# Kernel tuning notes

Measured on AMD Instinct MI355X. Metric: run time of the kernel, lower is better.

The kernel has to match this reference:

```python
import jax, jax.numpy as jnp
import numpy as np

N, D, E = 50000, 128, 800000


def setup_inputs() -> dict:
    key = jax.random.key(0)
    ks = jax.random.split(key, 12)
    s = 1.0 / np.sqrt(D)
    return {
        "x": jax.random.normal(ks[0], (N, D), jnp.float32),
        "edge_index": jax.random.randint(ks[1], (2, E), 0, N, jnp.int32),
        "W1": jax.random.normal(ks[2], (D, D), jnp.float32) * s,
        "bc1": jnp.zeros((D,), jnp.float32),
        "W2": jax.random.normal(ks[3], (D, D), jnp.float32) * s,
        "bc2": jnp.zeros((D,), jnp.float32),
        "w11": jax.random.normal(ks[4], (D, D), jnp.float32) * s,
        "w12": jax.random.normal(ks[5], (D, D), jnp.float32) * s,
        "b1": jax.random.uniform(ks[6], (D,), jnp.float32, -s, s),
        "w21": jax.random.normal(ks[7], (D, D), jnp.float32) * s,
        "w22": jax.random.normal(ks[8], (D, D), jnp.float32) * s,
        "b2": jax.random.uniform(ks[9], (D,), jnp.float32, -s, s),
    }


def gcn_conv(x, W, b, src, dst):
    """PyG GCNConv: self-loops + symmetric D^-1/2 (A+I) D^-1/2 normalization."""
    n = x.shape[0]
    h = x @ W  # [N, D]
    ones = jnp.ones(dst.shape[0], h.dtype)
    deg = jax.ops.segment_sum(ones, dst, num_segments=n) + 1.0  # +1 for self-loop
    dinv = jax.lax.rsqrt(deg)
    norm = dinv[src] * dinv[dst]  # [E]
    agg = jax.ops.segment_sum(h[src] * norm[:, None], dst, num_segments=n)
    agg = agg + h * (dinv * dinv)[:, None]  # self-loop messages
    return agg + b


def reference(x, edge_index, W1, bc1, W2, bc2, w11, w12, b1, w21, w22, b2):
    src, dst = edge_index[0], edge_index[1]
    # layer 1: forward and reversed edge directions (dropout is identity in eval)
    o1 = jax.nn.relu(gcn_conv(x, W1, bc1, src, dst))
    o2 = jax.nn.relu(gcn_conv(x, W1, bc1, dst, src))
    G = jax.nn.sigmoid(o1 @ w11.T + o2 @ w12.T + b1)
    h = G * o1 + (1.0 - G) * o2
    # layer 2
    p1 = jax.nn.relu(gcn_conv(h, W2, bc2, src, dst))
    p2 = jax.nn.relu(gcn_conv(h, W2, bc2, dst, src))
    G2 = jax.nn.sigmoid(p1 @ w21.T + p2 @ w22.T + b2)
    return G2 * p1 + (1.0 - G2) * p2
```

## Files before the change

kernel.cpp:

```cpp
#include <hip/hip_runtime.h>
#include <hip/hip_bf16.h>
#include <hip/hip_fp16.h>
#include <math.h>

#define D 128
#define SEG 4096
#define BSH 7
#define RCAP 4096
#define ACAP 4096
#define TRS 133

typedef _Float16 half8  __attribute__((ext_vector_type(8)));
typedef _Float16 half4v __attribute__((ext_vector_type(4)));
typedef float    fx4    __attribute__((ext_vector_type(4)));

__global__ __launch_bounds__(256) void scat2_kernel(const int* __restrict__ src,
                                                    const int* __restrict__ dst,
                                                    int e, int nb,
                                                    int* __restrict__ gcur1, int* __restrict__ gcur2,
                                                    unsigned int* __restrict__ rec1,
                                                    unsigned int* __restrict__ rec2) {
    __shared__ int h1[512], h2[512], o1[512], o2[512], run1[512], run2[512];
    int tid = threadIdx.x;
    for (int b = tid; b < nb; b += 256) { h1[b] = 0; h2[b] = 0; run1[b] = 0; run2[b] = 0; }
    __syncthreads();
    int s0 = blockIdx.x * SEG;
    int s1 = min(e, s0 + SEG);
    for (int idx = s0 + tid; idx < s1; idx += 256) {
        atomicAdd(&h1[dst[idx] >> BSH], 1);
        atomicAdd(&h2[src[idx] >> BSH], 1);
    }
    __syncthreads();
    for (int b = tid; b < nb; b += 256) {
        o1[b] = atomicAdd(&gcur1[b], h1[b]);
        o2[b] = atomicAdd(&gcur2[b], h2[b]);
    }
    __syncthreads();
    for (int idx = s0 + tid; idx < s1; idx += 256) {
        unsigned int sv = (unsigned int)src[idx];
        unsigned int dv = (unsigned int)dst[idx];
        int b1 = dv >> BSH, b2 = sv >> BSH;
        int p1 = o1[b1] + atomicAdd(&run1[b1], 1);
        if (p1 < RCAP) rec1[(size_t)b1 * RCAP + p1] = (dv << 16) | sv;
        int p2 = o2[b2] + atomicAdd(&run2[b2], 1);
        if (p2 < RCAP) rec2[(size_t)b2 * RCAP + p2] = (sv << 16) | dv;
    }
}

__global__ __launch_bounds__(256) void fin_kernel(const unsigned int* __restrict__ rec1,
                                                  const unsigned int* __restrict__ rec2,
                                                  const int* __restrict__ gcur1, const int* __restrict__ gcur2,
                                                  unsigned short* __restrict__ adj1, unsigned short* __restrict__ adj2,
                                                  int* __restrict__ ip1, int* __restrict__ ipe1,
                                                  int* __restrict__ ip2, int* __restrict__ ipe2,
                                                  float* __restrict__ dinv1, float* __restrict__ dinv2,
                                                  int n) {
    __shared__ unsigned int Lrec[RCAP];
    __shared__ unsigned short sadj[ACAP];
    __shared__ int deg[128], pscan[128], cur[128];
    __shared__ int ptot_s;
    int bkt = blockIdx.x;
    int dir = blockIdx.y;
    const unsigned int* rec = dir ? rec2 : rec1;
    const int* gc = dir ? gcur2 : gcur1;
    unsigned short* adj = dir ? adj2 : adj1;
    int* ip  = dir ? ip2 : ip1;
    int* ipe = dir ? ipe2 : ipe1;
    float* dinv = dir ? dinv2 : dinv1;

    int tid = threadIdx.x;
    int cnt = gc[bkt];
    if (cnt > RCAP) cnt = RCAP;
    size_t rbase = (size_t)bkt * RCAP;
    if (tid < 128) { deg[tid] = 0; cur[tid] = 0; }
    for (int i = tid; i < cnt; i += 256) Lrec[i] = rec[rbase + i];
    __syncthreads();
    int base = bkt << BSH;
    for (int i = tid; i < cnt; i += 256)
        atomicAdd(&deg[(int)(Lrec[i] >> 16) - base], 1);
    __syncthreads();
    if (tid < 128) pscan[tid] = (deg[tid] + 7) & ~7;
    __syncthreads();
    #pragma unroll
    for (int st = 1; st < 128; st <<= 1) {
        int add = (tid < 128 && tid >= st) ? pscan[tid - st] : 0;
        __syncthreads();
        if (tid < 128) pscan[tid] += add;
        __syncthreads();
    }
    if (tid == 127) ptot_s = min(pscan[127], ACAP);
    __syncthreads();
    int ptot = ptot_s;
    for (int i = tid; i < ptot; i += 256) sadj[i] = (unsigned short)n;
    __syncthreads();
    for (int i = tid; i < cnt; i += 256) {
        unsigned int r = Lrec[i];
        int l = (int)(r >> 16) - base;
        int pd = (deg[l] + 7) & ~7;
        int pos = pscan[l] - pd + atomicAdd(&cur[l], 1);
        if (pos < ACAP) sadj[pos] = (unsigned short)(r & 0xffffu);
    }
    __syncthreads();
    int gbase = bkt * ACAP;
    for (int i = tid; i < ptot; i += 256) adj[gbase + i] = sadj[i];
    if (tid < 128) {
        int node = base + tid;
        if (node < n) {
            int pd = (deg[tid] + 7) & ~7;
            ip[node]  = gbase + pscan[tid] - pd;
            ipe[node] = gbase + pscan[tid];
            dinv[node] = rsqrtf((float)deg[tid] + 1.0f);
        }
    }
    if (bkt == 0 && tid == 200) dinv[n] = 0.0f;
}

__global__ __launch_bounds__(256) void prep_kernel(const float* __restrict__ W1, const float* __restrict__ W2,
                                                   const float* __restrict__ w11, const float* __restrict__ w12,
                                                   const float* __restrict__ w21, const float* __restrict__ w22,
                                                   _Float16* __restrict__ T1, _Float16* __restrict__ T2,
                                                   _Float16* __restrict__ o11, _Float16* __restrict__ o12,
                                                   _Float16* __restrict__ o21, _Float16* __restrict__ o22) {
    __shared__ float s[32][33];
    int which = blockIdx.y;
    if (which < 2) {
        const float* w = which ? W2 : W1;
        _Float16* t = which ? T2 : T1;
        int tk = (blockIdx.x >> 2) * 32;
        int tc = (blockIdx.x & 3) * 32;
        int lr = threadIdx.x >> 5;
        int lc = threadIdx.x & 31;
        #pragma unroll
        for (int i = 0; i < 32; i += 8)
            s[lr + i][lc] = w[(size_t)(tk + lr + i) * D + tc + lc];
        __syncthreads();
        #pragma unroll
        for (int i = 0; i < 32; i += 8)
            t[(size_t)(tc + lr + i) * D + tk + lc] = (_Float16)s[lc][lr + i];
    } else {
        int wsel = which - 2;
        const float* w = (wsel == 0) ? w11 : (wsel == 1) ? w12 : (wsel == 2) ? w21 : w22;
        _Float16* o = (wsel == 0) ? o11 : (wsel == 1) ? o12 : (wsel == 2) ? o21 : o22;
        int idx = (blockIdx.x * 256 + threadIdx.x) * 4;
        float4 v = *(const float4*)&w[idx];
        half4v h = {(_Float16)v.x, (_Float16)v.y, (_Float16)v.z, (_Float16)v.w};
        *(half4v*)&o[idx] = h;
    }
}

__global__ __launch_bounds__(256) void gemm_f32a_kernel(const float* __restrict__ A,
                                                        const _Float16* __restrict__ Wt,
                                                        _Float16* __restrict__ C16, int n) {
    __shared__ float trs[4][16 * TRS];
    int tid = threadIdx.x;
    int wv = tid >> 6, lane = tid & 63;
    int m = lane & 15, q = lane >> 4;
    int row0 = blockIdx.x * 128 + wv * 32;
    size_t ar0 = (size_t)min(row0 + m, n - 1) * D;
    size_t ar1 = (size_t)min(row0 + 16 + m, n - 1) * D;
    fx4 acc[2][8];
    #pragma unroll
    for (int t = 0; t < 2; t++)
        #pragma unroll
        for (int ct = 0; ct < 8; ct++) acc[t][ct] = (fx4){0.f, 0.f, 0.f, 0.f};
    #pragma unroll
    for (int ks = 0; ks < 4; ks++) {
        int k0 = ks * 32 + q * 8;
        half8 bf[8];
        #pragma unroll
        for (int ct = 0; ct < 8; ct++)
            bf[ct] = *(const half8*)&Wt[(size_t)(ct * 16 + m) * D + k0];
        float4 u0 = *(const float4*)&A[ar0 + k0];
        float4 u1 = *(const float4*)&A[ar0 + k0 + 4];
        half8 a0 = {(_Float16)u0.x, (_Float16)u0.y, (_Float16)u0.z, (_Float16)u0.w,
                    (_Float16)u1.x, (_Float16)u1.y, (_Float16)u1.z, (_Float16)u1.w};
        float4 v0 = *(const float4*)&A[ar1 + k0];
        float4 v1 = *(const float4*)&A[ar1 + k0 + 4];
        half8 a1 = {(_Float16)v0.x, (_Float16)v0.y, (_Float16)v0.z, (_Float16)v0.w,
                    (_Float16)v1.x, (_Float16)v1.y, (_Float16)v1.z, (_Float16)v1.w};
        #pragma unroll
        for (int ct = 0; ct < 8; ct++) {
            acc[0][ct] = __builtin_amdgcn_mfma_f32_16x16x32_f16(a0, bf[ct], acc[0][ct], 0, 0, 0);
            acc[1][ct] = __builtin_amdgcn_mfma_f32_16x16x32_f16(a1, bf[ct], acc[1][ct], 0, 0, 0);
        }
    }
    float* Wl = trs[wv];
    #pragma unroll
    for (int t = 0; t < 2; t++) {
        #pragma unroll
        for (int reg = 0; reg < 4; reg++)
            #pragma unroll
            for (int ct = 0; ct < 8; ct++)
                Wl[(q * 4 + reg) * TRS + ct * 16 + m] = acc[t][ct][reg];
        int r = row0 + t * 16 + m;
        if (r < n) {
            size_t rr = (size_t)r * D;
            #pragma unroll
            for (int ks = 0; ks < 4; ks++) {
                int c0 = ks * 32 + q * 8;
                float4 p0 = *(const float4*)&Wl[m * TRS + c0];
                float4 p1 = *(const float4*)&Wl[m * TRS + c0 + 4];
                half8 hv = {(_Float16)p0.x, (_Float16)p0.y, (_Float16)p0.z, (_Float16)p0.w,
                            (_Float16)p1.x, (_Float16)p1.y, (_Float16)p1.z, (_Float16)p1.w};
                *(half8*)&C16[rr + c0] = hv;
            }
        }
    }
}

__global__ __launch_bounds__(256) void gemm_f16a_kernel(const _Float16* __restrict__ A,
                                                        const _Float16* __restrict__ Wt,
                                                        _Float16* __restrict__ C16, int n) {
    __shared__ float trs[4][16 * TRS];
    int tid = threadIdx.x;
    int wv = tid >> 6, lane = tid & 63;
    int m = lane & 15, q = lane >> 4;
    int row0 = blockIdx.x * 128 + wv * 32;
    size_t ar0 = (size_t)min(row0 + m, n - 1) * D;
    size_t ar1 = (size_t)min(row0 + 16 + m, n - 1) * D;
    fx4 acc[2][8];
    #pragma unroll
    for (int t = 0; t < 2; t++)
        #pragma unroll
        for (int ct = 0; ct < 8; ct++) acc[t][ct] = (fx4){0.f, 0.f, 0.f, 0.f};
    #pragma unroll
    for (int ks = 0; ks < 4; ks++) {
        int k0 = ks * 32 + q * 8;
        half8 bf[8];
        #pragma unroll
        for (int ct = 0; ct < 8; ct++)
            bf[ct] = *(const half8*)&Wt[(size_t)(ct * 16 + m) * D + k0];
        half8 a0 = *(const half8*)&A[ar0 + k0];
        half8 a1 = *(const half8*)&A[ar1 + k0];
        #pragma unroll
        for (int ct = 0; ct < 8; ct++) {
            acc[0][ct] = __builtin_amdgcn_mfma_f32_16x16x32_f16(a0, bf[ct], acc[0][ct], 0, 0, 0);
            acc[1][ct] = __builtin_amdgcn_mfma_f32_16x16x32_f16(a1, bf[ct], acc[1][ct], 0, 0, 0);
        }
    }
    float* Wl = trs[wv];
    #pragma unroll
    for (int t = 0; t < 2; t++) {
        #pragma unroll
        for (int reg = 0; reg < 4; reg++)
            #pragma unroll
            for (int ct = 0; ct < 8; ct++)
                Wl[(q * 4 + reg) * TRS + ct * 16 + m] = acc[t][ct][reg];
        int r = row0 + t * 16 + m;
        if (r < n) {
            size_t rr = (size_t)r * D;
            #pragma unroll
            for (int ks = 0; ks < 4; ks++) {
                int c0 = ks * 32 + q * 8;
                float4 p0 = *(const float4*)&Wl[m * TRS + c0];
                float4 p1 = *(const float4*)&Wl[m * TRS + c0 + 4];
                half8 hv = {(_Float16)p0.x, (_Float16)p0.y, (_Float16)p0.z, (_Float16)p0.w,
                            (_Float16)p1.x, (_Float16)p1.y, (_Float16)p1.z, (_Float16)p1.w};
                *(half8*)&C16[rr + c0] = hv;
            }
        }
    }
}

__global__ __launch_bounds__(256) void aggregate2_kernel(const __half* __restrict__ h16,
                                                         const int* __restrict__ ip1,
                                                         const int* __restrict__ ipe1,
                                                         const unsigned short* __restrict__ adj1,
                                                         const float* __restrict__ dinv1,
                                                         const int* __restrict__ ip2,
                                                         const int* __restrict__ ipe2,
                                                         const unsigned short* __restrict__ adj2,
                                                         const float* __restrict__ dinv2,
                                                         const float* __restrict__ bias,
                                                         _Float16* __restrict__ out1,
                                                         _Float16* __restrict__ out2, int n) {
    const int* ip  = blockIdx.y ? ip2 : ip1;
    const int* ipe = blockIdx.y ? ipe2 : ipe1;
    const unsigned short* adj = blockIdx.y ? adj2 : adj1;
    const float* dinv = blockIdx.y ? dinv2 : dinv1;
    _Float16* out = blockIdx.y ? out2 : out1;
    int wid = threadIdx.x >> 6, lane = threadIdx.x & 63;
    int half = lane >> 5, l32 = lane & 31;
    int i = blockIdx.x * 4 + wid;
    if (i >= n) return;
    int beg = ip[i], endp = ipe[i];
    int sh = half * 16;
    float4 acc = make_float4(0.f, 0.f, 0.f, 0.f);
    for (int j = beg; j < endp; j += 8) {
        uint4 av = *(const uint4*)&adj[j];
        int s0 = (av.x >> sh) & 0xffff;
        int s1 = (av.y >> sh) & 0xffff;
        int s2 = (av.z >> sh) & 0xffff;
        int s3 = (av.w >> sh) & 0xffff;
        float w0 = dinv[s0], w1 = dinv[s1], w2 = dinv[s2], w3 = dinv[s3];
        uint2 r0 = *(const uint2*)&h16[(size_t)s0 * D + 4 * l32];
        uint2 r1 = *(const uint2*)&h16[(size_t)s1 * D + 4 * l32];
        uint2 r2 = *(const uint2*)&h16[(size_t)s2 * D + 4 * l32];
        uint2 r3 = *(const uint2*)&h16[(size_t)s3 * D + 4 * l32];
        float2 a0 = __half22float2(*(__half2*)&r0.x), b0 = __half22float2(*(__half2*)&r0.y);
        float2 a1 = __half22float2(*(__half2*)&r1.x), b1 = __half22float2(*(__half2*)&r1.y);
        float2 a2 = __half22float2(*(__half2*)&r2.x), b2 = __half22float2(*(__half2*)&r2.y);
        float2 a3 = __half22float2(*(__half2*)&r3.x), b3 = __half22float2(*(__half2*)&r3.y);
        acc.x += w0 * a0.x + w1 * a1.x + w2 * a2.x + w3 * a3.x;
        acc.y += w0 * a0.y + w1 * a1.y + w2 * a2.y + w3 * a3.y;
        acc.z += w0 * b0.x + w1 * b1.x + w2 * b2.x + w3 * b3.x;
        acc.w += w0 * b0.y + w1 * b1.y + w2 * b2.y + w3 * b3.y;
    }
    acc.x += __shfl_xor(acc.x, 32, 64);
    acc.y += __shfl_xor(acc.y, 32, 64);
    acc.z += __shfl_xor(acc.z, 32, 64);
    acc.w += __shfl_xor(acc.w, 32, 64);
    if (half == 0) {
        float di = dinv[i];
        float d2 = di * di;
        uint2 rs = *(const uint2*)&h16[(size_t)i * D + 4 * l32];
        float2 s0 = __half22float2(*(__half2*)&rs.x);
        float2 s1 = __half22float2(*(__half2*)&rs.y);
        float4 bv = *(const float4*)&bias[4 * l32];
        half4v o;
        o[0] = (_Float16)fmaxf(di * acc.x + d2 * s0.x + bv.x, 0.f);
        o[1] = (_Float16)fmaxf(di * acc.y + d2 * s0.y + bv.y, 0.f);
        o[2] = (_Float16)fmaxf(di * acc.z + d2 * s1.x + bv.z, 0.f);
        o[3] = (_Float16)fmaxf(di * acc.w + d2 * s1.y + bv.w, 0.f);
        *(half4v*)&out[(size_t)i * D + 4 * l32] = o;
    }
}

__global__ __launch_bounds__(256) void gate_mfma_kernel(const _Float16* __restrict__ o1,
                                                        const _Float16* __restrict__ o2,
                                                        const _Float16* __restrict__ w1,
                                                        const _Float16* __restrict__ w2,
                                                        const float* __restrict__ b,
                                                        float* __restrict__ out32,
                                                        _Float16* __restrict__ out16,
                                                        int write16, int n) {
    __shared__ float trs[4][16 * TRS];
    int tid = threadIdx.x;
    int wv = tid >> 6, lane = tid & 63;
    int m = lane & 15, q = lane >> 4;
    int row0 = blockIdx.x * 128 + wv * 32;
    size_t ar0 = (size_t)min(row0 + m, n - 1) * D;
    size_t ar1 = (size_t)min(row0 + 16 + m, n - 1) * D;
    fx4 acc[2][8];
    #pragma unroll
    for (int t = 0; t < 2; t++)
        #pragma unroll
        for (int ct = 0; ct < 8; ct++) acc[t][ct] = (fx4){0.f, 0.f, 0.f, 0.f};
    #pragma unroll
    for (int ks = 0; ks < 4; ks++) {
        int k0 = ks * 32 + q * 8;
        half8 bf1[8], bf2[8];
        #pragma unroll
        for (int ct = 0; ct < 8; ct++) {
            bf1[ct] = *(const half8*)&w1[(size_t)(ct * 16 + m) * D + k0];
            bf2[ct] = *(const half8*)&w2[(size_t)(ct * 16 + m) * D + k0];
        }
        half8 a10 = *(const half8*)&o1[ar0 + k0];
        half8 a20 = *(const half8*)&o2[ar0 + k0];
        half8 a11 = *(const half8*)&o1[ar1 + k0];
        half8 a21 = *(const half8*)&o2[ar1 + k0];
        #pragma unroll
        for (int ct = 0; ct < 8; ct++) {
            acc[0][ct] = __builtin_amdgcn_mfma_f32_16x16x32_f16(a10, bf1[ct], acc[0][ct], 0, 0, 0);
            acc[0][ct] = __builtin_amdgcn_mfma_f32_16x16x32_f16(a20, bf2[ct], acc[0][ct], 0, 0, 0);
            acc[1][ct] = __builtin_amdgcn_mfma_f32_16x16x32_f16(a11, bf1[ct], acc[1][ct], 0, 0, 0);
            acc[1][ct] = __builtin_amdgcn_mfma_f32_16x16x32_f16(a21, bf2[ct], acc[1][ct], 0, 0, 0);
        }
    }
    float bb[4][8];
    #pragma unroll
    for (int ks = 0; ks < 4; ks++) {
        float4 b0 = *(const float4*)&b[ks * 32 + q * 8];
        float4 b1 = *(const float4*)&b[ks * 32 + q * 8 + 4];
        bb[ks][0] = b0.x; bb[ks][1] = b0.y; bb[ks][2] = b0.z; bb[ks][3] = b0.w;
        bb[ks][4] = b1.x; bb[ks][5] = b1.y; bb[ks][6] = b1.z; bb[ks][7] = b1.w;
    }
    float* Wl = trs[wv];
    #pragma unroll
    for (int t = 0; t < 2; t++) {
        #pragma unroll
        for (int reg = 0; reg < 4; reg++)
            #pragma unroll
            for (int ct = 0; ct < 8; ct++)
                Wl[(q * 4 + reg) * TRS + ct * 16 + m] = acc[t][ct][reg];
        int r = row0 + t * 16 + m;
        size_t rr = (size_t)min(r, n - 1) * D;
        #pragma unroll
        for (int ks = 0; ks < 4; ks++) {
            int c0 = ks * 32 + q * 8;
            float4 p0 = *(const float4*)&Wl[m * TRS + c0];
            float4 p1 = *(const float4*)&Wl[m * TRS + c0 + 4];
            half8 u1 = *(const half8*)&o1[rr + c0];
            half8 u2 = *(const half8*)&o2[rr + c0];
            float pv[8] = {p0.x, p0.y, p0.z, p0.w, p1.x, p1.y, p1.z, p1.w};
            float res[8];
            #pragma unroll
            for (int j = 0; j < 8; j++) {
                float tv = pv[j] + bb[ks][j];
                float g = 1.0f / (1.0f + __expf(-tv));
                res[j] = g * (float)u1[j] + (1.0f - g) * (float)u2[j];
            }
            if (r < n) {
                if (write16) {
                    half8 hv = {(_Float16)res[0], (_Float16)res[1], (_Float16)res[2], (_Float16)res[3],
                                (_Float16)res[4], (_Float16)res[5], (_Float16)res[6], (_Float16)res[7]};
                    *(half8*)&out16[rr + c0] = hv;
                } else {
                    *(float4*)&out32[rr + c0]     = make_float4(res[0], res[1], res[2], res[3]);
                    *(float4*)&out32[rr + c0 + 4] = make_float4(res[4], res[5], res[6], res[7]);
                }
            }
        }
    }
}

extern "C" void kernel_launch(void* const* d_in, const int* in_sizes, int n_in,
                              void* d_out, int out_size, void* d_ws, size_t ws_size,
                              hipStream_t stream) {
    const float* x   = (const float*)d_in[0];
    const int*   eix = (const int*)d_in[1];
    const float* W1  = (const float*)d_in[2];
    const float* bc1 = (const float*)d_in[3];
    const float* W2  = (const float*)d_in[4];
    const float* bc2 = (const float*)d_in[5];
    const float* w11 = (const float*)d_in[6];
    const float* w12 = (const float*)d_in[7];
    const float* b1  = (const float*)d_in[8];
    const float* w21 = (const float*)d_in[9];
    const float* w22 = (const float*)d_in[10];
    const float* b2  = (const float*)d_in[11];
    int n = in_sizes[0] / D;
    int e = in_sizes[1] / 2;
    const int* src = eix;
    const int* dst = eix + e;

    int nb = (n + 127) >> BSH;
    int nblk = (e + SEG - 1) / SEG;

    char* p = (char*)d_ws;
    auto alloc = [&](size_t bytes) {
        char* q = p;
        p += (bytes + 255) & ~(size_t)255;
        return q;
    };
    int* gcur1 = (int*)alloc((size_t)2 * 512 * sizeof(int));
    int* gcur2 = gcur1 + 512;
    unsigned int* rec1 = (unsigned int*)alloc((size_t)nb * RCAP * sizeof(unsigned int));
    unsigned int* rec2 = (unsigned int*)alloc((size_t)nb * RCAP * sizeof(unsigned int));
    int*   ip1   = (int*)alloc((size_t)n * sizeof(int));
    int*   ipe1  = (int*)alloc((size_t)n * sizeof(int));
    int*   ip2   = (int*)alloc((size_t)n * sizeof(int));
    int*   ipe2  = (int*)alloc((size_t)n * sizeof(int));
    float* dinv1 = (float*)alloc((size_t)(n + 1) * sizeof(float));
    float* dinv2 = (float*)alloc((size_t)(n + 1) * sizeof(float));
    unsigned short* adj1 = (unsigned short*)alloc((size_t)nb * ACAP * sizeof(unsigned short));
    unsigned short* adj2 = (unsigned short*)alloc((size_t)nb * ACAP * sizeof(unsigned short));
    _Float16* W1t  = (_Float16*)alloc((size_t)D * D * sizeof(_Float16));
    _Float16* W2t  = (_Float16*)alloc((size_t)D * D * sizeof(_Float16));
    _Float16* w11h = (_Float16*)alloc((size_t)D * D * sizeof(_Float16));
    _Float16* w12h = (_Float16*)alloc((size_t)D * D * sizeof(_Float16));
    _Float16* w21h = (_Float16*)alloc((size_t)D * D * sizeof(_Float16));
    _Float16* w22h = (_Float16*)alloc((size_t)D * D * sizeof(_Float16));
    _Float16* h16  = (_Float16*)alloc((size_t)(n + 1) * D * sizeof(_Float16));
    _Float16* o1h  = (_Float16*)alloc((size_t)n * D * sizeof(_Float16));
    _Float16* o2h  = (_Float16*)alloc((size_t)n * D * sizeof(_Float16));
    _Float16* h2h  = (_Float16*)alloc((size_t)n * D * sizeof(_Float16));
    float* outF  = (float*)d_out;

    hipMemsetAsync(gcur1, 0, (size_t)2 * 512 * sizeof(int), stream);
    prep_kernel<<<dim3(16, 6), 256, 0, stream>>>(W1, W2, w11, w12, w21, w22,
                                                 W1t, W2t, w11h, w12h, w21h, w22h);
    scat2_kernel<<<nblk, 256, 0, stream>>>(src, dst, e, nb, gcur1, gcur2, rec1, rec2);
    fin_kernel<<<dim3(nb, 2), 256, 0, stream>>>(rec1, rec2, gcur1, gcur2,
                                                adj1, adj2, ip1, ipe1, ip2, ipe2, dinv1, dinv2, n);

    int gG = (n + 127) / 128;
    int gA = (n + 3) / 4;
    gemm_f32a_kernel<<<gG, 256, 0, stream>>>(x, W1t, h16, n);
    aggregate2_kernel<<<dim3(gA, 2), 256, 0, stream>>>((const __half*)h16,
                                                       ip1, ipe1, adj1, dinv1,
                                                       ip2, ipe2, adj2, dinv2,
                                                       bc1, o1h, o2h, n);
    gate_mfma_kernel<<<gG, 256, 0, stream>>>(o1h, o2h, w11h, w12h, b1,
                                             nullptr, h2h, 1, n);
    gemm_f16a_kernel<<<gG, 256, 0, stream>>>(h2h, W2t, h16, n);
    aggregate2_kernel<<<dim3(gA, 2), 256, 0, stream>>>((const __half*)h16,
                                                       ip1, ipe1, adj1, dinv1,
                                                       ip2, ipe2, adj2, dinv2,
                                                       bc2, o1h, o2h, n);
    gate_mfma_kernel<<<gG, 256, 0, stream>>>(o1h, o2h, w21h, w22h, b2,
                                             outF, nullptr, 0, n);
}
```

Baseline: 330.6 us.

## Precompute per-edge weights, fuse gate with second GEMM, restructure aggregation

Degrees are now counted globally with atomics in the scatter kernel, and the finalize kernel stores a per-edge source normalization weight next to the adjacency, so aggregation no longer does a random dinv lookup per neighbour. The layer-1 gate kernel is fused with the layer-2 feature GEMM, which removes the h2 round trip and one kernel launch. The aggregation loop now software-prefetches the next group of indices and weights, splits the work by halves of the neighbour list per half-wave, and writes its output with both half-waves active. In exchange it adds global atomics over all edges, an extra float array per edge that must be read, and more registers in the fused kernel.

```diff
diff --git a/kernel.cpp b/kernel.cpp
--- a/kernel.cpp
+++ b/kernel.cpp
@@ -18,6 +18,7 @@
                                                     const int* __restrict__ dst,
                                                     int e, int nb,
                                                     int* __restrict__ gcur1, int* __restrict__ gcur2,
+                                                    int* __restrict__ deg1g, int* __restrict__ deg2g,
                                                     unsigned int* __restrict__ rec1,
                                                     unsigned int* __restrict__ rec2) {
     __shared__ int h1[512], h2[512], o1[512], o2[512], run1[512], run2[512];
@@ -27,8 +28,11 @@
     int s0 = blockIdx.x * SEG;
     int s1 = min(e, s0 + SEG);
     for (int idx = s0 + tid; idx < s1; idx += 256) {
-        atomicAdd(&h1[dst[idx] >> BSH], 1);
-        atomicAdd(&h2[src[idx] >> BSH], 1);
+        int dv = dst[idx], sv = src[idx];
+        atomicAdd(&h1[dv >> BSH], 1);
+        atomicAdd(&h2[sv >> BSH], 1);
+        atomicAdd(&deg1g[dv], 1);
+        atomicAdd(&deg2g[sv], 1);
     }
     __syncthreads();
     for (int b = tid; b < nb; b += 256) {
@@ -50,20 +54,25 @@
 __global__ __launch_bounds__(256) void fin_kernel(const unsigned int* __restrict__ rec1,
                                                   const unsigned int* __restrict__ rec2,
                                                   const int* __restrict__ gcur1, const int* __restrict__ gcur2,
+                                                  const int* __restrict__ deg1g, const int* __restrict__ deg2g,
                                                   unsigned short* __restrict__ adj1, unsigned short* __restrict__ adj2,
+                                                  float* __restrict__ wf1, float* __restrict__ wf2,
                                                   int* __restrict__ ip1, int* __restrict__ ipe1,
                                                   int* __restrict__ ip2, int* __restrict__ ipe2,
                                                   float* __restrict__ dinv1, float* __restrict__ dinv2,
                                                   int n) {
     __shared__ unsigned int Lrec[RCAP];
     __shared__ unsigned short sadj[ACAP];
+    __shared__ float swf[ACAP];
     __shared__ int deg[128], pscan[128], cur[128];
     __shared__ int ptot_s;
     int bkt = blockIdx.x;
     int dir = blockIdx.y;
     const unsigned int* rec = dir ? rec2 : rec1;
     const int* gc = dir ? gcur2 : gcur1;
+    const int* degG = dir ? deg2g : deg1g;
     unsigned short* adj = dir ? adj2 : adj1;
+    float* wf = dir ? wf2 : wf1;
     int* ip  = dir ? ip2 : ip1;
     int* ipe = dir ? ipe2 : ipe1;
     float* dinv = dir ? dinv2 : dinv1;
@@ -72,12 +81,13 @@
     int cnt = gc[bkt];
     if (cnt > RCAP) cnt = RCAP;
     size_t rbase = (size_t)bkt * RCAP;
-    if (tid < 128) { deg[tid] = 0; cur[tid] = 0; }
+    int base = bkt << BSH;
+    if (tid < 128) {
+        int node = base + tid;
+        deg[tid] = (node < n) ? degG[node] : 0;
+        cur[tid] = 0;
+    }
     for (int i = tid; i < cnt; i += 256) Lrec[i] = rec[rbase + i];
-    __syncthreads();
-    int base = bkt << BSH;
-    for (int i = tid; i < cnt; i += 256)
-        atomicAdd(&deg[(int)(Lrec[i] >> 16) - base], 1);
     __syncthreads();
     if (tid < 128) pscan[tid] = (deg[tid] + 7) & ~7;
     __syncthreads();
@@ -91,18 +101,22 @@
     if (tid == 127) ptot_s = min(pscan[127], ACAP);
     __syncthreads();
     int ptot = ptot_s;
-    for (int i = tid; i < ptot; i += 256) sadj[i] = (unsigned short)n;
+    for (int i = tid; i < ptot; i += 256) { sadj[i] = (unsigned short)n; swf[i] = 0.0f; }
     __syncthreads();
     for (int i = tid; i < cnt; i += 256) {
         unsigned int r = Lrec[i];
         int l = (int)(r >> 16) - base;
+        int sid = (int)(r & 0xffffu);
         int pd = (deg[l] + 7) & ~7;
         int pos = pscan[l] - pd + atomicAdd(&cur[l], 1);
-        if (pos < ACAP) sadj[pos] = (unsigned short)(r & 0xffffu);
+        if (pos < ACAP) {
+            sadj[pos] = (unsigned short)sid;
+            swf[pos] = rsqrtf((float)degG[sid] + 1.0f);
+        }
     }
     __syncthreads();
     int gbase = bkt * ACAP;
-    for (int i = tid; i < ptot; i += 256) adj[gbase + i] = sadj[i];
+    for (int i = tid; i < ptot; i += 256) { adj[gbase + i] = sadj[i]; wf[gbase + i] = swf[i]; }
     if (tid < 128) {
         int node = base + tid;
         if (node < n) {
@@ -112,7 +126,6 @@
             dinv[node] = rsqrtf((float)deg[tid] + 1.0f);
         }
     }
-    if (bkt == 0 && tid == 200) dinv[n] = 0.0f;
 }
 
 __global__ __launch_bounds__(256) void prep_kernel(const float* __restrict__ W1, const float* __restrict__ W2,
@@ -208,9 +221,86 @@
     }
 }
 
-__global__ __launch_bounds__(256) void gemm_f16a_kernel(const _Float16* __restrict__ A,
-                                                        const _Float16* __restrict__ Wt,
-                                                        _Float16* __restrict__ C16, int n) {
+__global__ __launch_bounds__(256) void aggregate2_kernel(const __half* __restrict__ h16,
+                                                         const int* __restrict__ ip1,
+                                                         const int* __restrict__ ipe1,
+                                                         const unsigned short* __restrict__ adj1,
+                                                         const float* __restrict__ wf1,
+                                                         const float* __restrict__ dinv1,
+                                                         const int* __restrict__ ip2,
+                                                         const int* __restrict__ ipe2,
+                                                         const unsigned short* __restrict__ adj2,
+                                                         const float* __restrict__ wf2,
+                                                         const float* __restrict__ dinv2,
+                                                         const float* __restrict__ bias,
+                                                         _Float16* __restrict__ out1,
+                                                         _Float16* __restrict__ out2, int n) {
+    const int* ip  = blockIdx.y ? ip2 : ip1;
+    const int* ipe = blockIdx.y ? ipe2 : ipe1;
+    const unsigned short* adj = blockIdx.y ? adj2 : adj1;
+    const float* wf = blockIdx.y ? wf2 : wf1;
+    const float* dinv = blockIdx.y ? dinv2 : dinv1;
+    _Float16* out = blockIdx.y ? out2 : out1;
+    int wid = threadIdx.x >> 6, lane = threadIdx.x & 63;
+    int hf = lane >> 5, l32 = lane & 31;
+    int i = blockIdx.x * 4 + wid;
+    if (i >= n) return;
+    int beg = ip[i], endp = ipe[i];
+    int fcol = 4 * l32;
+    float4 acc = make_float4(0.f, 0.f, 0.f, 0.f);
+    if (beg < endp) {
+        int hoff = hf << 2;
+        int j = beg;
+        uint2  iv = *(const uint2*)&adj[j + hoff];
+        float4 wv = *(const float4*)&wf[j + hoff];
+        while (true) {
+            int jn = j + 8;
+            int jp = jn < endp ? jn : j;
+            uint2  niv = *(const uint2*)&adj[jp + hoff];
+            float4 nwv = *(const float4*)&wf[jp + hoff];
+            int s0 = iv.x & 0xffff, s1 = iv.x >> 16;
+            int s2 = iv.y & 0xffff, s3 = iv.y >> 16;
+            uint2 r0 = *(const uint2*)&h16[(s0 << 7) + fcol];
+            uint2 r1 = *(const uint2*)&h16[(s1 << 7) + fcol];
+            uint2 r2 = *(const uint2*)&h16[(s2 << 7) + fcol];
+            uint2 r3 = *(const uint2*)&h16[(s3 << 7) + fcol];
+            float2 a0 = __half22float2(*(__half2*)&r0.x), b0 = __half22float2(*(__half2*)&r0.y);
+            float2 a1 = __half22float2(*(__half2*)&r1.x), b1 = __half22float2(*(__half2*)&r1.y);
+            float2 a2 = __half22float2(*(__half2*)&r2.x), b2 = __half22float2(*(__half2*)&r2.y);
+            float2 a3 = __half22float2(*(__half2*)&r3.x), b3 = __half22float2(*(__half2*)&r3.y);
+            acc.x += wv.x * a0.x + wv.y * a1.x + wv.z * a2.x + wv.w * a3.x;
+            acc.y += wv.x * a0.y + wv.y * a1.y + wv.z * a2.y + wv.w * a3.y;
+            acc.z += wv.x * b0.x + wv.y * b1.x + wv.z * b2.x + wv.w * b3.x;
+            acc.w += wv.x * b0.y + wv.y * b1.y + wv.z * b2.y + wv.w * b3.y;
+            if (jn >= endp) break;
+            iv = niv; wv = nwv; j = jn;
+        }
+    }
+    acc.x += __shfl_xor(acc.x, 32, 64);
+    acc.y += __shfl_xor(acc.y, 32, 64);
+    acc.z += __shfl_xor(acc.z, 32, 64);
+    acc.w += __shfl_xor(acc.w, 32, 64);
+    float di = dinv[i];
+    float d2 = di * di;
+    float ax = hf ? acc.z : acc.x;
+    float ay = hf ? acc.w : acc.y;
+    int off = (i << 7) + fcol + 2 * hf;
+    unsigned int rs = *(const unsigned int*)&h16[off];
+    float2 sv = __half22float2(*(const __half2*)&rs);
+    float2 bv = *(const float2*)&bias[fcol + 2 * hf];
+    float r0f = fmaxf(di * ax + d2 * sv.x + bv.x, 0.f);
+    float r1f = fmaxf(di * ay + d2 * sv.y + bv.y, 0.f);
+    __half2 hv = __floats2half2_rn(r0f, r1f);
+    *(__half2*)&out[off] = hv;
+}
+
+__global__ __launch_bounds__(256) void gate_gemm_kernel(const _Float16* __restrict__ o1,
+                                                        const _Float16* __restrict__ o2,
+                                                        const _Float16* __restrict__ w1,
+                                                        const _Float16* __restrict__ w2,
+                                                        const float* __restrict__ b,
+                                                        const _Float16* __restrict__ Wt2,
+                                                        _Float16* __restrict__ hh, int n) {
     __shared__ float trs[4][16 * TRS];
     int tid = threadIdx.x;
     int wv = tid >> 6, lane = tid & 63;
@@ -226,18 +316,33 @@
     #pragma unroll
     for (int ks = 0; ks < 4; ks++) {
         int k0 = ks * 32 + q * 8;
-        half8 bf[8];
-        #pragma unroll
-        for (int ct = 0; ct < 8; ct++)
-            bf[ct] = *(const half8*)&Wt[(size_t)(ct * 16 + m) * D + k0];
-        half8 a0 = *(const half8*)&A[ar0 + k0];
-        half8 a1 = *(const half8*)&A[ar1 + k0];
+        half8 bf1[8], bf2[8];
         #pragma unroll
         for (int ct = 0; ct < 8; ct++) {
-            acc[0][ct] = __builtin_amdgcn_mfma_f32_16x16x32_f16(a0, bf[ct], acc[0][ct], 0, 0, 0);
-            acc[1][ct] = __builtin_amdgcn_mfma_f32_16x16x32_f16(a1, bf[ct], acc[1][ct], 0, 0, 0);
-        }
-    }
+            bf1[ct] = *(const half8*)&w1[(size_t)(ct * 16 + m) * D + k0];
+            bf2[ct] = *(const half8*)&w2[(size_t)(ct * 16 + m) * D + k0];
+        }
+        half8 a10 = *(const half8*)&o1[ar0 + k0];
+        half8 a20 = *(const half8*)&o2[ar0 + k0];
+        half8 a11 = *(const half8*)&o1[ar1 + k0];
+        half8 a21 = *(const half8*)&o2[ar1 + k0];
+        #pragma unroll
+        for (int ct = 0; ct < 8; ct++) {
+            acc[0][ct] = __builtin_amdgcn_mfma_f32_16x16x32_f16(a10, bf1[ct], acc[0][ct], 0, 0, 0);
+            acc[0][ct] = __builtin_amdgcn_mfma_f32_16x16x32_f16(a20, bf2[ct], acc[0][ct], 0, 0, 0);
+            acc[1][ct] = __builtin_amdgcn_mfma_f32_16x16x32_f16(a11, bf1[ct], acc[1][ct], 0, 0, 0);
+            acc[1][ct] = __builtin_amdgcn_mfma_f32_16x16x32_f16(a21, bf2[ct], acc[1][ct], 0, 0, 0);
+        }
+    }
+    float bb[4][8];
+    #pragma unroll
+    for (int ks = 0; ks < 4; ks++) {
+        float4 b0 = *(const float4*)&b[ks * 32 + q * 8];
+        float4 b1 = *(const float4*)&b[ks * 32 + q * 8 + 4];
+        bb[ks][0] = b0.x; bb[ks][1] = b0.y; bb[ks][2] = b0.z; bb[ks][3] = b0.w;
+        bb[ks][4] = b1.x; bb[ks][5] = b1.y; bb[ks][6] = b1.z; bb[ks][7] = b1.w;
+    }
+    half8 resf[2][4];
     float* Wl = trs[wv];
     #pragma unroll
     for (int t = 0; t < 2; t++) {
@@ -246,6 +351,50 @@
             #pragma unroll
             for (int ct = 0; ct < 8; ct++)
                 Wl[(q * 4 + reg) * TRS + ct * 16 + m] = acc[t][ct][reg];
+        size_t rr = (size_t)min(row0 + t * 16 + m, n - 1) * D;
+        #pragma unroll
+        for (int ks = 0; ks < 4; ks++) {
+            int c0 = ks * 32 + q * 8;
+            float4 p0 = *(const float4*)&Wl[m * TRS + c0];
+            float4 p1 = *(const float4*)&Wl[m * TRS + c0 + 4];
+            half8 u1 = *(const half8*)&o1[rr + c0];
+            half8 u2 = *(const half8*)&o2[rr + c0];
+            float pv[8] = {p0.x, p0.y, p0.z, p0.w, p1.x, p1.y, p1.z, p1.w};
+            half8 hv;
+            #pragma unroll
+            for (int jj = 0; jj < 8; jj++) {
+                float tv = pv[jj] + bb[ks][jj];
+                float g = 1.0f / (1.0f + __expf(-tv));
+                hv[jj] = (_Float16)(g * (float)u1[jj] + (1.0f - g) * (float)u2[jj]);
+            }
+            resf[t][ks] = hv;
+        }
+    }
+    fx4 acc2[2][8];
+    #pragma unroll
+    for (int t = 0; t < 2; t++)
+        #pragma unroll
+        for (int ct = 0; ct < 8; ct++) acc2[t][ct] = (fx4){0.f, 0.f, 0.f, 0.f};
+    #pragma unroll
+    for (int ks = 0; ks < 4; ks++) {
+        int k0 = ks * 32 + q * 8;
+        half8 bf[8];
+        #pragma unroll
+        for (int ct = 0; ct < 8; ct++)
+            bf[ct] = *(const half8*)&Wt2[(size_t)(ct * 16 + m) * D + k0];
+        #pragma unroll
+        for (int ct = 0; ct < 8; ct++) {
+            acc2[0][ct] = __builtin_amdgcn_mfma_f32_16x16x32_f16(resf[0][ks], bf[ct], acc2[0][ct], 0, 0, 0);
+            acc2[1][ct] = __builtin_amdgcn_mfma_f32_16x16x32_f16(resf[1][ks], bf[ct], acc2[1][ct], 0, 0, 0);
+        }
+    }
+    #pragma unroll
+    for (int t = 0; t < 2; t++) {
+        #pragma unroll
+        for (int reg = 0; reg < 4; reg++)
+            #pragma unroll
+            for (int ct = 0; ct < 8; ct++)
+                Wl[(q * 4 + reg) * TRS + ct * 16 + m] = acc2[t][ct][reg];
         int r = row0 + t * 16 + m;
         if (r < n) {
             size_t rr = (size_t)r * D;
@@ -256,73 +405,9 @@
                 float4 p1 = *(const float4*)&Wl[m * TRS + c0 + 4];
                 half8 hv = {(_Float16)p0.x, (_Float16)p0.y, (_Float16)p0.z, (_Float16)p0.w,
                             (_Float16)p1.x, (_Float16)p1.y, (_Float16)p1.z, (_Float16)p1.w};
-                *(half8*)&C16[rr + c0] = hv;
+                *(half8*)&hh[rr + c0] = hv;
             }
         }
-    }
-}
-
-__global__ __launch_bounds__(256) void aggregate2_kernel(const __half* __restrict__ h16,
-                                                         const int* __restrict__ ip1,
-                                                         const int* __restrict__ ipe1,
-                                                         const unsigned short* __restrict__ adj1,
-                                                         const float* __restrict__ dinv1,
-                                                         const int* __restrict__ ip2,
-                                                         const int* __restrict__ ipe2,
-                                                         const unsigned short* __restrict__ adj2,
-                                                         const float* __restrict__ dinv2,
-                                                         const float* __restrict__ bias,
-                                                         _Float16* __restrict__ out1,
-                                                         _Float16* __restrict__ out2, int n) {
-    const int* ip  = blockIdx.y ? ip2 : ip1;
-    const int* ipe = blockIdx.y ? ipe2 : ipe1;
-    const unsigned short* adj = blockIdx.y ? adj2 : adj1;
-    const float* dinv = blockIdx.y ? dinv2 : dinv1;
-    _Float16* out = blockIdx.y ? out2 : out1;
-    int wid = threadIdx.x >> 6, lane = threadIdx.x & 63;
-    int half = lane >> 5, l32 = lane & 31;
-    int i = blockIdx.x * 4 + wid;
-    if (i >= n) return;
-    int beg = ip[i], endp = ipe[i];
-    int sh = half * 16;
-    float4 acc = make_float4(0.f, 0.f, 0.f, 0.f);
-    for (int j = beg; j < endp; j += 8) {
-        uint4 av = *(const uint4*)&adj[j];
-        int s0 = (av.x >> sh) & 0xffff;
-        int s1 = (av.y >> sh) & 0xffff;
-        int s2 = (av.z >> sh) & 0xffff;
-        int s3 = (av.w >> sh) & 0xffff;
-        float w0 = dinv[s0], w1 = dinv[s1], w2 = dinv[s2], w3 = dinv[s3];
-        uint2 r0 = *(const uint2*)&h16[(size_t)s0 * D + 4 * l32];
-        uint2 r1 = *(const uint2*)&h16[(size_t)s1 * D + 4 * l32];
-        uint2 r2 = *(const uint2*)&h16[(size_t)s2 * D + 4 * l32];
-        uint2 r3 = *(const uint2*)&h16[(size_t)s3 * D + 4 * l32];
-        float2 a0 = __half22float2(*(__half2*)&r0.x), b0 = __half22float2(*(__half2*)&r0.y);
-        float2 a1 = __half22float2(*(__half2*)&r1.x), b1 = __half22float2(*(__half2*)&r1.y);
-        float2 a2 = __half22float2(*(__half2*)&r2.x), b2 = __half22float2(*(__half2*)&r2.y);
-        float2 a3 = __half22float2(*(__half2*)&r3.x), b3 = __half22float2(*(__half2*)&r3.y);
-        acc.x += w0 * a0.x + w1 * a1.x + w2 * a2.x + w3 * a3.x;
-        acc.y += w0 * a0.y + w1 * a1.y + w2 * a2.y + w3 * a3.y;
-        acc.z += w0 * b0.x + w1 * b1.x + w2 * b2.x + w3 * b3.x;
-        acc.w += w0 * b0.y + w1 * b1.y + w2 * b2.y + w3 * b3.y;
-    }
-    acc.x += __shfl_xor(acc.x, 32, 64);
-    acc.y += __shfl_xor(acc.y, 32, 64);
-    acc.z += __shfl_xor(acc.z, 32, 64);
-    acc.w += __shfl_xor(acc.w, 32, 64);
-    if (half == 0) {
-        float di = dinv[i];
-        float d2 = di * di;
-        uint2 rs = *(const uint2*)&h16[(size_t)i * D + 4 * l32];
-        float2 s0 = __half22float2(*(__half2*)&rs.x);
-        float2 s1 = __half22float2(*(__half2*)&rs.y);
-        float4 bv = *(const float4*)&bias[4 * l32];
-        half4v o;
-        o[0] = (_Float16)fmaxf(di * acc.x + d2 * s0.x + bv.x, 0.f);
-        o[1] = (_Float16)fmaxf(di * acc.y + d2 * s0.y + bv.y, 0.f);
-        o[2] = (_Float16)fmaxf(di * acc.z + d2 * s1.x + bv.z, 0.f);
-        o[3] = (_Float16)fmaxf(di * acc.w + d2 * s1.y + bv.w, 0.f);
-        *(half4v*)&out[(size_t)i * D + 4 * l32] = o;
     }
 }
 
@@ -331,9 +416,7 @@
                                                         const _Float16* __restrict__ w1,
                                                         const _Float16* __restrict__ w2,
                                                         const float* __restrict__ b,
-                                                        float* __restrict__ out32,
-                                                        _Float16* __restrict__ out16,
-                                                        int write16, int n) {
+                                                        float* __restrict__ out32, int n) {
     __shared__ float trs[4][16 * TRS];
     int tid = threadIdx.x;
     int wv = tid >> 6, lane = tid & 63;
@@ -401,14 +484,8 @@
                 res[j] = g * (float)u1[j] + (1.0f - g) * (float)u2[j];
             }
             if (r < n) {
-                if (write16) {
-                    half8 hv = {(_Float16)res[0], (_Float16)res[1], (_Float16)res[2], (_Float16)res[3],
-                                (_Float16)res[4], (_Float16)res[5], (_Float16)res[6], (_Float16)res[7]};
-                    *(half8*)&out16[rr + c0] = hv;
-                } else {
-                    *(float4*)&out32[rr + c0]     = make_float4(res[0], res[1], res[2], res[3]);
-                    *(float4*)&out32[rr + c0 + 4] = make_float4(res[4], res[5], res[6], res[7]);
-                }
+                *(float4*)&out32[rr + c0]     = make_float4(res[0], res[1], res[2], res[3]);
+                *(float4*)&out32[rr + c0 + 4] = make_float4(res[4], res[5], res[6], res[7]);
             }
         }
     }
@@ -443,8 +520,10 @@
         p += (bytes + 255) & ~(size_t)255;
         return q;
     };
-    int* gcur1 = (int*)alloc((size_t)2 * 512 * sizeof(int));
+    int* gcur1 = (int*)alloc((size_t)(1024 + 2 * n) * sizeof(int));
     int* gcur2 = gcur1 + 512;
+    int* deg1g = gcur1 + 1024;
+    int* deg2g = deg1g + n;
     unsigned int* rec1 = (unsigned int*)alloc((size_t)nb * RCAP * sizeof(unsigned int));
     unsigned int* rec2 = (unsigned int*)alloc((size_t)nb * RCAP * sizeof(unsigned int));
     int*   ip1   = (int*)alloc((size_t)n * sizeof(int));
@@ -455,6 +534,8 @@
     float* dinv2 = (float*)alloc((size_t)(n + 1) * sizeof(float));
     unsigned short* adj1 = (unsigned short*)alloc((size_t)nb * ACAP * sizeof(unsigned short));
     unsigned short* adj2 = (unsigned short*)alloc((size_t)nb * ACAP * sizeof(unsigned short));
+    float* wf1 = (float*)alloc((size_t)nb * ACAP * sizeof(float));
+    float* wf2 = (float*)alloc((size_t)nb * ACAP * sizeof(float));
     _Float16* W1t  = (_Float16*)alloc((size_t)D * D * sizeof(_Float16));
     _Float16* W2t  = (_Float16*)alloc((size_t)D * D * sizeof(_Float16));
     _Float16* w11h = (_Float16*)alloc((size_t)D * D * sizeof(_Float16));
@@ -464,30 +545,28 @@
     _Float16* h16  = (_Float16*)alloc((size_t)(n + 1) * D * sizeof(_Float16));
     _Float16* o1h  = (_Float16*)alloc((size_t)n * D * sizeof(_Float16));
     _Float16* o2h  = (_Float16*)alloc((size_t)n * D * sizeof(_Float16));
-    _Float16* h2h  = (_Float16*)alloc((size_t)n * D * sizeof(_Float16));
     float* outF  = (float*)d_out;
 
-    hipMemsetAsync(gcur1, 0, (size_t)2 * 512 * sizeof(int), stream);
+    hipMemsetAsync(gcur1, 0, (size_t)(1024 + 2 * n) * sizeof(int), stream);
+    hipMemsetAsync(h16 + (size_t)n * D, 0, D * sizeof(_Float16), stream);
     prep_kernel<<<dim3(16, 6), 256, 0, stream>>>(W1, W2, w11, w12, w21, w22,
                                                  W1t, W2t, w11h, w12h, w21h, w22h);
-    scat2_kernel<<<nblk, 256, 0, stream>>>(src, dst, e, nb, gcur1, gcur2, rec1, rec2);
-    fin_kernel<<<dim3(nb, 2), 256, 0, stream>>>(rec1, rec2, gcur1, gcur2,
-                                                adj1, adj2, ip1, ipe1, ip2, ipe2, dinv1, dinv2, n);
+    scat2_kernel<<<nblk, 256, 0, stream>>>(src, dst, e, nb, gcur1, gcur2, deg1g, deg2g, rec1, rec2);
+    fin_kernel<<<dim3(nb, 2), 256, 0, stream>>>(rec1, rec2, gcur1, gcur2, deg1g, deg2g,
+                                                adj1, adj2, wf1, wf2,
+                                                ip1, ipe1, ip2, ipe2, dinv1, dinv2, n);
 
     int gG = (n + 127) / 128;
     int gA = (n + 3) / 4;
     gemm_f32a_kernel<<<gG, 256, 0, stream>>>(x, W1t, h16, n);
     aggregate2_kernel<<<dim3(gA, 2), 256, 0, stream>>>((const __half*)h16,
-                                                       ip1, ipe1, adj1, dinv1,
-                                                       ip2, ipe2, adj2, dinv2,
+                                                       ip1, ipe1, adj1, wf1, dinv1,
+                                                       ip2, ipe2, adj2, wf2, dinv2,
                                                        bc1, o1h, o2h, n);
-    gate_mfma_kernel<<<gG, 256, 0, stream>>>(o1h, o2h, w11h, w12h, b1,
-                                             nullptr, h2h, 1, n);
-    gemm_f16a_kernel<<<gG, 256, 0, stream>>>(h2h, W2t, h16, n);
+    gate_gemm_kernel<<<gG, 256, 0, stream>>>(o1h, o2h, w11h, w12h, b1, W2t, h16, n);
     aggregate2_kernel<<<dim3(gA, 2), 256, 0, stream>>>((const __half*)h16,
-                                                       ip1, ipe1, adj1, dinv1,
-                                                       ip2, ipe2, adj2, dinv2,
+                                                       ip1, ipe1, adj1, wf1, dinv1,
+                                                       ip2, ipe2, adj2, wf2, dinv2,
                                                        bc2, o1h, o2h, n);
-    gate_mfma_kernel<<<gG, 256, 0, stream>>>(o1h, o2h, w21h, w22h, b2,
-                                             outF, nullptr, 0, n);
-}
+    gate_mfma_kernel<<<gG, 256, 0, stream>>>(o1h, o2h, w21h, w22h, b2, outF, n);
+}
```

New measurement: 397.7 us. 1.2x slower.
